# Kernel tuning notes

Hardware: AMD Instinct MI355X
Metric: run time of the kernel (lower is better)

Reference implementation:

```python
import jax, jax.numpy as jnp
import numpy as np

N = 50000      # nodes
E = 640000     # edges (before self loops)
IN = 128       # in_channels
H = 4          # heads (layer 1)
C = 64         # hidden_channels per head
OUT = 64       # out_channels
SLOPE = 0.2    # PyG GATConv default negative_slope


def setup_inputs() -> dict:
    key = jax.random.key(0)
    ks = jax.random.split(key, 12)
    x = jax.random.normal(ks[0], (N, IN), dtype=jnp.float32)
    edge_src = jax.random.randint(ks[1], (E,), 0, N, dtype=jnp.int32)
    edge_dst = jax.random.randint(ks[2], (E,), 0, N, dtype=jnp.int32)
    # Layer 1 params: Linear IN -> H*C, attention vectors a_src/a_dst [H, C], bias [H*C]
    W1 = jax.random.normal(ks[3], (IN, H * C), dtype=jnp.float32) / np.sqrt(IN)
    att_src1 = jax.random.normal(ks[4], (H, C), dtype=jnp.float32) / np.sqrt(C)
    att_dst1 = jax.random.normal(ks[5], (H, C), dtype=jnp.float32) / np.sqrt(C)
    b1 = jnp.zeros((H * C,), dtype=jnp.float32)
    # Layer 2 params: Linear H*C -> OUT, 1 head
    W2 = jax.random.normal(ks[6], (H * C, OUT), dtype=jnp.float32) / np.sqrt(H * C)
    att_src2 = jax.random.normal(ks[7], (1, OUT), dtype=jnp.float32) / np.sqrt(OUT)
    att_dst2 = jax.random.normal(ks[8], (1, OUT), dtype=jnp.float32) / np.sqrt(OUT)
    b2 = jnp.zeros((OUT,), dtype=jnp.float32)
    return {"x": x, "W1": W1, "att_src1": att_src1, "att_dst1": att_dst1, "b1": b1,
            "W2": W2, "att_src2": att_src2, "att_dst2": att_dst2, "b2": b2,
            "edge_src": edge_src, "edge_dst": edge_dst}


def gat_conv(x, src, dst, W, a_src, a_dst, b, heads, ch):
    """PyG GATConv (concat=True): gather -> LeakyReLU attention -> per-dst softmax -> scatter-add."""
    n = x.shape[0]
    h = (x @ W).reshape(n, heads, ch)                  # [N, H, C]
    al_s = jnp.sum(h * a_src, axis=-1)                 # [N, H] node-level src attention term
    al_d = jnp.sum(h * a_dst, axis=-1)                 # [N, H]
    e = jax.nn.leaky_relu(al_s[src] + al_d[dst], SLOPE)  # [E, H] edge scores
    m = jax.ops.segment_max(e, dst, num_segments=n)    # stable per-dst softmax
    ex = jnp.exp(e - m[dst])
    den = jax.ops.segment_sum(ex, dst, num_segments=n)
    alpha = ex / den[dst]                              # [E, H]
    msg = h[src] * alpha[:, :, None]                   # [E, H, C]
    out = jax.ops.segment_sum(msg, dst, num_segments=n)  # [N, H, C]
    return out.reshape(n, heads * ch) + b


def reference(x, W1, att_src1, att_dst1, b1, W2, att_src2, att_dst2, b2, edge_src, edge_dst):
    # PyG GATConv default add_self_loops=True
    loops = jnp.arange(N, dtype=edge_src.dtype)
    src = jnp.concatenate([edge_src, loops])
    dst = jnp.concatenate([edge_dst, loops])
    h = gat_conv(x, src, dst, W1, att_src1, att_dst1, b1, H, C)
    h = jax.nn.elu(h)                                  # F.elu; dropout p=0 -> no-op
    out = gat_conv(h, src, dst, W2, att_src2, att_dst2, b2, 1, OUT)
    return out
```

## Files before the change

kernel.cpp:

```cpp
#include <hip/hip_runtime.h>
#include <hip/hip_bf16.h>
#include <cstdint>
#include <cstddef>

#define N_NODES 50000
#define N_EDGES 640000
#define ET (N_EDGES + N_NODES)
#define IN_CH 128
#define H1 4
#define HC1 256
#define OUT_CH 64
#define SLOPE 0.2f
#define SCAN_NBLK ((N_NODES + 255) / 256)

typedef __attribute__((ext_vector_type(8))) short short8;
typedef __attribute__((ext_vector_type(4))) float floatx4;

__device__ __forceinline__ float bf2f(unsigned short u) {
    return __uint_as_float(((unsigned)u) << 16);
}
__device__ __forceinline__ unsigned short f2bf(float f) {
    unsigned u = __float_as_uint(f);
    unsigned r = 0x7fffu + ((u >> 16) & 1u);
    return (unsigned short)((u + r) >> 16);
}
__device__ __forceinline__ float ldf(const void* p, size_t i, bool f32) {
    return f32 ? ((const float*)p)[i] : bf2f(((const unsigned short*)p)[i]);
}

__global__ void detect_dtype(const unsigned short* __restrict__ x, unsigned* __restrict__ flag) {
    int lane = threadIdx.x & 63;
    int bad = 0;
    #pragma unroll
    for (int r = 0; r < 4; ++r) {
        float v = bf2f(x[r * 64 + lane]);
        if (!(v == v) || fabsf(v) > 1e4f) bad = 1;
    }
    unsigned long long m = __ballot(bad != 0);
    if (lane == 0) *flag = (m != 0ull) ? 1u : 0u;
}

#define XW (N_NODES * IN_CH / 8)
#define W1N (IN_CH * HC1)
#define W2N (HC1 * OUT_CH)
__global__ void conv_all(const void* __restrict__ x, const void* __restrict__ W1,
                         const void* __restrict__ W2, const unsigned* __restrict__ flag,
                         unsigned short* __restrict__ x16,
                         unsigned short* __restrict__ Wt1, unsigned short* __restrict__ Wt2)
{
    int i = blockIdx.x * blockDim.x + threadIdx.x;
    const bool f32 = (*flag != 0);
    if (i < XW) {
        size_t off = (size_t)i * 8;
        uint4 st;
        if (f32) {
            const float* xp = (const float*)x + off;
            float4 a = *(const float4*)xp;
            float4 b = *(const float4*)(xp + 4);
            st.x = (unsigned)f2bf(a.x) | ((unsigned)f2bf(a.y) << 16);
            st.y = (unsigned)f2bf(a.z) | ((unsigned)f2bf(a.w) << 16);
            st.z = (unsigned)f2bf(b.x) | ((unsigned)f2bf(b.y) << 16);
            st.w = (unsigned)f2bf(b.z) | ((unsigned)f2bf(b.w) << 16);
        } else {
            st = *(const uint4*)((const unsigned short*)x + off);
        }
        *(uint4*)(x16 + off) = st;
    } else if (i < XW + W1N) {
        int j = i - XW;
        int n = j / IN_CH, k = j % IN_CH;
        Wt1[j] = f2bf(ldf(W1, (size_t)k * HC1 + n, f32));
    } else if (i < XW + W1N + W2N) {
        int j = i - XW - W1N;
        int n = j / HC1, k = j % HC1;
        Wt2[j] = f2bf(ldf(W2, (size_t)k * OUT_CH + n, f32));
    }
}

__global__ void count_edges(const int* __restrict__ edst, int* __restrict__ counts)
{
    int i = blockIdx.x * blockDim.x + threadIdx.x;
    if (i >= ET) return;
    int d = (i < N_EDGES) ? edst[i] : (i - N_EDGES);
    atomicAdd(&counts[d], 1);
}

__global__ __launch_bounds__(256) void block_sums(
    const int* __restrict__ counts, int* __restrict__ bsum)
{
    int i = blockIdx.x * 256 + threadIdx.x;
    int v = (i < N_NODES) ? counts[i] : 0;
    #pragma unroll
    for (int off = 32; off > 0; off >>= 1) v += __shfl_down(v, off, 64);
    __shared__ int ws[4];
    int lane = threadIdx.x & 63, w = threadIdx.x >> 6;
    if (lane == 0) ws[w] = v;
    __syncthreads();
    if (threadIdx.x == 0) bsum[blockIdx.x] = ws[0] + ws[1] + ws[2] + ws[3];
}

__global__ __launch_bounds__(256) void scan_block_sums(
    const int* __restrict__ bsum, int* __restrict__ boff)
{
    __shared__ int s[256];
    int t = threadIdx.x;
    int v = (t < SCAN_NBLK) ? bsum[t] : 0;
    s[t] = v;
    __syncthreads();
    #pragma unroll
    for (int off = 1; off < 256; off <<= 1) {
        int u = (t >= off) ? s[t - off] : 0;
        __syncthreads();
        s[t] += u;
        __syncthreads();
    }
    if (t < SCAN_NBLK) boff[t] = s[t] - v;
}

__global__ __launch_bounds__(256) void write_rowptr(
    const int* __restrict__ counts, const int* __restrict__ boff,
    int* __restrict__ rowptr, int* __restrict__ cursor)
{
    __shared__ int s[256];
    int t = threadIdx.x;
    int i = blockIdx.x * 256 + t;
    int v = (i < N_NODES) ? counts[i] : 0;
    s[t] = v;
    __syncthreads();
    #pragma unroll
    for (int off = 1; off < 256; off <<= 1) {
        int u = (t >= off) ? s[t - off] : 0;
        __syncthreads();
        s[t] += u;
        __syncthreads();
    }
    if (i < N_NODES) {
        int r = boff[blockIdx.x] + s[t] - v;
        rowptr[i] = r; cursor[i] = r;
    }
    if (i == 0) rowptr[N_NODES] = ET;
}

__global__ void fill_csr(const int* __restrict__ esrc, const int* __restrict__ edst,
                         int* __restrict__ cursor, int* __restrict__ ecsr)
{
    int i = blockIdx.x * blockDim.x + threadIdx.x;
    if (i >= ET) return;
    int s = (i < N_EDGES) ? esrc[i] : (i - N_EDGES);
    int d = (i < N_EDGES) ? edst[i] : (i - N_EDGES);
    int pos = atomicAdd(&cursor[d], 1);
    ecsr[pos] = s;
}

template <int KK>
__global__ __launch_bounds__(256) void gemm_fused(
    const unsigned short* __restrict__ A,
    const unsigned short* __restrict__ Bt,
    const void* __restrict__ avs, const void* __restrict__ avd,
    const unsigned* __restrict__ flag,
    unsigned short* __restrict__ C,
    float* __restrict__ als, float* __restrict__ ald,
    int M, int N)
{
    const int tid = threadIdx.x;
    const int m0 = blockIdx.y * 64, n0 = blockIdx.x * 64;
    const int w = tid >> 6, lane = tid & 63;
    const int ln = lane & 15, quad = lane >> 4;
    const int m_frag = m0 + w * 16 + ln;
    floatx4 acc[4] = {{0.f,0.f,0.f,0.f},{0.f,0.f,0.f,0.f},{0.f,0.f,0.f,0.f},{0.f,0.f,0.f,0.f}};

    #pragma unroll
    for (int ks = 0; ks < KK / 32; ++ks) {
        const int kbase = ks * 32 + quad * 8;
        short8 a;
        if (m_frag < M) {
            a = *(const short8*)(A + (size_t)m_frag * KK + kbase);
        } else {
            #pragma unroll
            for (int j = 0; j < 8; ++j) a[j] = 0;
        }
        #pragma unroll
        for (int sub = 0; sub < 4; ++sub) {
            short8 b = *(const short8*)(Bt + (size_t)(n0 + sub * 16 + ln) * KK + kbase);
            acc[sub] = __builtin_amdgcn_mfma_f32_16x16x32_bf16(a, b, acc[sub], 0, 0, 0);
        }
    }

    #pragma unroll
    for (int sub = 0; sub < 4; ++sub) {
        #pragma unroll
        for (int r = 0; r < 4; ++r) {
            int m = m0 + w * 16 + quad * 4 + r;
            if (m < M)
                C[(size_t)m * N + n0 + sub * 16 + ln] = f2bf(acc[sub][r]);
        }
    }

    const bool f32in = (*flag != 0);
    float as[4], av[4];
    #pragma unroll
    for (int sub = 0; sub < 4; ++sub) {
        as[sub] = ldf(avs, n0 + sub * 16 + ln, f32in);
        av[sub] = ldf(avd, n0 + sub * 16 + ln, f32in);
    }
    const int Hh = N >> 6;
    #pragma unroll
    for (int r = 0; r < 4; ++r) {
        float ps = 0.f, pd = 0.f;
        #pragma unroll
        for (int sub = 0; sub < 4; ++sub) {
            ps += acc[sub][r] * as[sub];
            pd += acc[sub][r] * av[sub];
        }
        #pragma unroll
        for (int off = 1; off < 16; off <<= 1) {
            ps += __shfl_xor(ps, off, 64);
            pd += __shfl_xor(pd, off, 64);
        }
        int m = m0 + w * 16 + quad * 4 + r;
        if (ln == 0 && m < M) {
            als[(size_t)m * Hh + blockIdx.x] = ps;
            ald[(size_t)m * Hh + blockIdx.x] = pd;
        }
    }
}

__global__ __launch_bounds__(256) void agg_node1(
    const int* __restrict__ rowptr, const int* __restrict__ ecsr,
    const unsigned short* __restrict__ h, const float* __restrict__ als,
    const float* __restrict__ ald, const void* __restrict__ bias,
    const unsigned* __restrict__ flag, unsigned short* __restrict__ out)
{
    int wave = (blockIdx.x * blockDim.x + threadIdx.x) >> 6;
    int lane = threadIdx.x & 63;
    if (wave >= N_NODES) return;
    const int d = wave;
    const int hg = lane >> 4;
    const int c0 = (lane & 15) << 2;
    const int lo = rowptr[d], hi = rowptr[d + 1];
    const float ad = ald[d * H1 + hg];

    float acc0 = 0.f, acc1 = 0.f, acc2 = 0.f, acc3 = 0.f, den = 0.f;

    for (int eb = lo; eb < hi; eb += 8) {
        int s[8]; uint2 q[8]; float p[8];
        #pragma unroll
        for (int j = 0; j < 8; ++j) {
            int e = eb + j;
            s[j] = ecsr[(e < hi) ? e : (hi - 1)];
        }
        #pragma unroll
        for (int j = 0; j < 8; ++j)
            q[j] = *(const uint2*)(h + (size_t)s[j] * HC1 + hg * 64 + c0);
        #pragma unroll
        for (int j = 0; j < 8; ++j) {
            float t = als[s[j] * H1 + hg] + ad;
            t = (t > 0.f) ? t : SLOPE * t;
            float pv = __expf(t);
            p[j] = (eb + j < hi) ? pv : 0.f;
        }
        #pragma unroll
        for (int j = 0; j < 8; ++j) {
            den  += p[j];
            acc0 += p[j] * __uint_as_float(q[j].x << 16);
            acc1 += p[j] * __uint_as_float(q[j].x & 0xffff0000u);
            acc2 += p[j] * __uint_as_float(q[j].y << 16);
            acc3 += p[j] * __uint_as_float(q[j].y & 0xffff0000u);
        }
    }

    const bool f32in = (*flag != 0);
    const float inv = 1.f / den;
    float v0 = acc0 * inv + ldf(bias, hg * 64 + c0 + 0, f32in);
    float v1 = acc1 * inv + ldf(bias, hg * 64 + c0 + 1, f32in);
    float v2 = acc2 * inv + ldf(bias, hg * 64 + c0 + 2, f32in);
    float v3 = acc3 * inv + ldf(bias, hg * 64 + c0 + 3, f32in);
    v0 = (v0 > 0.f) ? v0 : (__expf(v0) - 1.f);
    v1 = (v1 > 0.f) ? v1 : (__expf(v1) - 1.f);
    v2 = (v2 > 0.f) ? v2 : (__expf(v2) - 1.f);
    v3 = (v3 > 0.f) ? v3 : (__expf(v3) - 1.f);
    uint2 st;
    st.x = (unsigned)f2bf(v0) | ((unsigned)f2bf(v1) << 16);
    st.y = (unsigned)f2bf(v2) | ((unsigned)f2bf(v3) << 16);
    *(uint2*)(out + (size_t)d * HC1 + hg * 64 + c0) = st;
}

__global__ __launch_bounds__(256) void agg_node2(
    const int* __restrict__ rowptr, const int* __restrict__ ecsr,
    const unsigned short* __restrict__ h, const float* __restrict__ als,
    const float* __restrict__ ald, const void* __restrict__ bias,
    const unsigned* __restrict__ flag, float* __restrict__ out)
{
    int wave = (blockIdx.x * blockDim.x + threadIdx.x) >> 6;
    int lane = threadIdx.x & 63;
    if (wave >= N_NODES) return;
    const int d = wave;
    const int eg = lane >> 3;
    const int c0 = (lane & 7) << 3;
    const int lo = rowptr[d], hi = rowptr[d + 1];
    const float ad = ald[d];

    float acc[8];
    #pragma unroll
    for (int j = 0; j < 8; ++j) acc[j] = 0.f;
    float den = 0.f;

    for (int eb = lo; eb < hi; eb += 8) {
        int e = eb + eg;
        if (e < hi) {
            int s = ecsr[e];
            uint4 q = *(const uint4*)(h + (size_t)s * OUT_CH + c0);
            float t = als[s] + ad;
            t = (t > 0.f) ? t : SLOPE * t;
            float p = __expf(t);
            den += p;
            acc[0] += p * __uint_as_float(q.x << 16);
            acc[1] += p * __uint_as_float(q.x & 0xffff0000u);
            acc[2] += p * __uint_as_float(q.y << 16);
            acc[3] += p * __uint_as_float(q.y & 0xffff0000u);
            acc[4] += p * __uint_as_float(q.z << 16);
            acc[5] += p * __uint_as_float(q.z & 0xffff0000u);
            acc[6] += p * __uint_as_float(q.w << 16);
            acc[7] += p * __uint_as_float(q.w & 0xffff0000u);
        }
    }
    #pragma unroll
    for (int off = 8; off <= 32; off <<= 1) {
        den += __shfl_xor(den, off, 64);
        #pragma unroll
        for (int j = 0; j < 8; ++j) acc[j] += __shfl_xor(acc[j], off, 64);
    }
    if (lane < 8) {
        const bool f32in = (*flag != 0);
        const float inv = 1.f / den;
        float4 v0, v1;
        v0.x = acc[0] * inv + ldf(bias, c0 + 0, f32in);
        v0.y = acc[1] * inv + ldf(bias, c0 + 1, f32in);
        v0.z = acc[2] * inv + ldf(bias, c0 + 2, f32in);
        v0.w = acc[3] * inv + ldf(bias, c0 + 3, f32in);
        v1.x = acc[4] * inv + ldf(bias, c0 + 4, f32in);
        v1.y = acc[5] * inv + ldf(bias, c0 + 5, f32in);
        v1.z = acc[6] * inv + ldf(bias, c0 + 6, f32in);
        v1.w = acc[7] * inv + ldf(bias, c0 + 7, f32in);
        *(float4*)(out + (size_t)d * OUT_CH + c0) = v0;
        *(float4*)(out + (size_t)d * OUT_CH + c0 + 4) = v1;
    }
}

extern "C" void kernel_launch(void* const* d_in, const int* in_sizes, int n_in,
                              void* d_out, int out_size, void* d_ws, size_t ws_size,
                              hipStream_t stream)
{
    const void* x   = d_in[0];
    const void* W1  = d_in[1];
    const void* as1 = d_in[2];
    const void* ad1 = d_in[3];
    const void* b1  = d_in[4];
    const void* W2  = d_in[5];
    const void* as2 = d_in[6];
    const void* ad2 = d_in[7];
    const void* b2  = d_in[8];
    const int* esrc = (const int*)d_in[9];
    const int* edst = (const int*)d_in[10];
    float* out = (float*)d_out;

    char* base = (char*)d_ws;
    const size_t MB = 1024 * 1024;
    unsigned short* x16  = (unsigned short*)(base);
    unsigned short* h16  = (unsigned short*)(base + 13 * MB);
    unsigned short* xo16 = (unsigned short*)(base + 39 * MB);
    unsigned short* h2   = (unsigned short*)(base + 65 * MB);
    float* als    = (float*)(base + 72 * MB);
    float* ald    = (float*)(base + 73 * MB);
    unsigned short* Wt1 = (unsigned short*)(base + 74 * MB);
    unsigned short* Wt2 = (unsigned short*)(base + 75 * MB);
    int* counts   = (int*)(base + 76 * MB);
    int* rowptr   = (int*)(base + 77 * MB);
    int* cursor   = (int*)(base + 78 * MB);
    int* ecsr     = (int*)(base + 79 * MB);
    int* bsum     = (int*)(base + 82 * MB);
    int* boff     = bsum + 256;
    unsigned* flag = (unsigned*)(base + 83 * MB);

    const int BLK = 256;
    const int edge_blocks = (ET + BLK - 1) / BLK;
    const int node_wave_blocks = (N_NODES * 64 + BLK - 1) / BLK;
    const int mtiles = (N_NODES + 63) / 64;

    detect_dtype<<<1, 64, 0, stream>>>((const unsigned short*)x, flag);

    (void)hipMemsetAsync(counts, 0, N_NODES * sizeof(int), stream);
    count_edges<<<edge_blocks, BLK, 0, stream>>>(edst, counts);
    block_sums<<<SCAN_NBLK, BLK, 0, stream>>>(counts, bsum);
    scan_block_sums<<<1, BLK, 0, stream>>>(bsum, boff);
    write_rowptr<<<SCAN_NBLK, BLK, 0, stream>>>(counts, boff, rowptr, cursor);
    fill_csr<<<edge_blocks, BLK, 0, stream>>>(esrc, edst, cursor, ecsr);

    conv_all<<<(XW + W1N + W2N + BLK - 1) / BLK, BLK, 0, stream>>>(
        x, W1, W2, flag, x16, Wt1, Wt2);

    {
        dim3 g(HC1 / 64, mtiles);
        gemm_fused<IN_CH><<<g, BLK, 0, stream>>>(x16, Wt1, as1, ad1, flag, h16, als, ald, N_NODES, HC1);
    }
    agg_node1<<<node_wave_blocks, BLK, 0, stream>>>(
        rowptr, ecsr, h16, als, ald, b1, flag, xo16);

    {
        dim3 g(OUT_CH / 64, mtiles);
        gemm_fused<HC1><<<g, BLK, 0, stream>>>(xo16, Wt2, as2, ad2, flag, h2, als, ald, N_NODES, OUT_CH);
    }
    agg_node2<<<node_wave_blocks, BLK, 0, stream>>>(
        rowptr, ecsr, h2, als, ald, b2, flag, out);
}
```

Baseline: 307.8 us.

## Merge preprocessing kernels and fold scan into one pass with inter-block spin

Cuts the launch count by merging independent work into shared grids. Dtype detection and the counts zeroing go into one init kernel, x/weight conversion is fused with edge counting, and the CSR fill is fused with the first GEMM. The three scan kernels become a single kernel where block 0 waits on an atomic counter, scans the block sums and releases the other blocks through a flag, which relies on all 196 blocks being co-resident. The layer-1 aggregation loop also changes from 8-wide clamped batches to 4-wide exact batches plus a scalar tail, dropping the wasted padded loads at the cost of less memory-level parallelism per iteration.

```diff
diff --git a/kernel.cpp b/kernel.cpp
--- a/kernel.cpp
+++ b/kernel.cpp
@@ -12,6 +12,13 @@
 #define OUT_CH 64
 #define SLOPE 0.2f
 #define SCAN_NBLK ((N_NODES + 255) / 256)
+#define XW (N_NODES * IN_CH / 8)
+#define W1N (IN_CH * HC1)
+#define W2N (HC1 * OUT_CH)
+#define CONVB ((XW + W1N + W2N + 255) / 256)
+#define EDGEB ((ET + 255) / 256)
+#define MT ((N_NODES + 63) / 64)
+#define G1B (4 * MT)
 
 typedef __attribute__((ext_vector_type(8))) short short8;
 typedef __attribute__((ext_vector_type(4))) float floatx4;
@@ -28,82 +35,84 @@
     return f32 ? ((const float*)p)[i] : bf2f(((const unsigned short*)p)[i]);
 }
 
-__global__ void detect_dtype(const unsigned short* __restrict__ x, unsigned* __restrict__ flag) {
-    int lane = threadIdx.x & 63;
-    int bad = 0;
-    #pragma unroll
-    for (int r = 0; r < 4; ++r) {
-        float v = bf2f(x[r * 64 + lane]);
-        if (!(v == v) || fabsf(v) > 1e4f) bad = 1;
-    }
-    unsigned long long m = __ballot(bad != 0);
-    if (lane == 0) *flag = (m != 0ull) ? 1u : 0u;
-}
-
-#define XW (N_NODES * IN_CH / 8)
-#define W1N (IN_CH * HC1)
-#define W2N (HC1 * OUT_CH)
-__global__ void conv_all(const void* __restrict__ x, const void* __restrict__ W1,
-                         const void* __restrict__ W2, const unsigned* __restrict__ flag,
-                         unsigned short* __restrict__ x16,
-                         unsigned short* __restrict__ Wt1, unsigned short* __restrict__ Wt2)
-{
-    int i = blockIdx.x * blockDim.x + threadIdx.x;
-    const bool f32 = (*flag != 0);
-    if (i < XW) {
-        size_t off = (size_t)i * 8;
-        uint4 st;
-        if (f32) {
-            const float* xp = (const float*)x + off;
-            float4 a = *(const float4*)xp;
-            float4 b = *(const float4*)(xp + 4);
-            st.x = (unsigned)f2bf(a.x) | ((unsigned)f2bf(a.y) << 16);
-            st.y = (unsigned)f2bf(a.z) | ((unsigned)f2bf(a.w) << 16);
-            st.z = (unsigned)f2bf(b.x) | ((unsigned)f2bf(b.y) << 16);
-            st.w = (unsigned)f2bf(b.z) | ((unsigned)f2bf(b.w) << 16);
-        } else {
-            st = *(const uint4*)((const unsigned short*)x + off);
-        }
-        *(uint4*)(x16 + off) = st;
-    } else if (i < XW + W1N) {
-        int j = i - XW;
-        int n = j / IN_CH, k = j % IN_CH;
-        Wt1[j] = f2bf(ldf(W1, (size_t)k * HC1 + n, f32));
-    } else if (i < XW + W1N + W2N) {
-        int j = i - XW - W1N;
-        int n = j / HC1, k = j % HC1;
-        Wt2[j] = f2bf(ldf(W2, (size_t)k * OUT_CH + n, f32));
-    }
-}
-
-__global__ void count_edges(const int* __restrict__ edst, int* __restrict__ counts)
-{
-    int i = blockIdx.x * blockDim.x + threadIdx.x;
-    if (i >= ET) return;
-    int d = (i < N_EDGES) ? edst[i] : (i - N_EDGES);
-    atomicAdd(&counts[d], 1);
-}
-
-__global__ __launch_bounds__(256) void block_sums(
-    const int* __restrict__ counts, int* __restrict__ bsum)
-{
-    int i = blockIdx.x * 256 + threadIdx.x;
+__global__ __launch_bounds__(256) void init_all(
+    const unsigned short* __restrict__ x, unsigned* __restrict__ flag,
+    int* __restrict__ counts, int* __restrict__ state)
+{
+    int b = blockIdx.x;
+    if (b < SCAN_NBLK) {
+        int i = b * 256 + threadIdx.x;
+        if (i < N_NODES) counts[i] = 0;
+    } else {
+        int t = threadIdx.x;
+        if (t < 64) {
+            int bad = 0;
+            #pragma unroll
+            for (int r = 0; r < 4; ++r) {
+                float v = bf2f(x[r * 64 + t]);
+                if (!(v == v) || fabsf(v) > 1e4f) bad = 1;
+            }
+            unsigned long long m = __ballot(bad != 0);
+            if (t == 0) *flag = (m != 0ull) ? 1u : 0u;
+        } else if (t == 64) {
+            state[0] = 0; state[1] = 0;
+        }
+    }
+}
+
+__global__ __launch_bounds__(256) void conv_count(
+    const void* __restrict__ x, const void* __restrict__ W1,
+    const void* __restrict__ W2, const unsigned* __restrict__ flag,
+    unsigned short* __restrict__ x16,
+    unsigned short* __restrict__ Wt1, unsigned short* __restrict__ Wt2,
+    const int* __restrict__ edst, int* __restrict__ counts)
+{
+    int b = blockIdx.x;
+    if (b < CONVB) {
+        int i = b * 256 + threadIdx.x;
+        const bool f32 = (*flag != 0);
+        if (i < XW) {
+            size_t off = (size_t)i * 8;
+            uint4 st;
+            if (f32) {
+                const float* xp = (const float*)x + off;
+                float4 a = *(const float4*)xp;
+                float4 c = *(const float4*)(xp + 4);
+                st.x = (unsigned)f2bf(a.x) | ((unsigned)f2bf(a.y) << 16);
+                st.y = (unsigned)f2bf(a.z) | ((unsigned)f2bf(a.w) << 16);
+                st.z = (unsigned)f2bf(c.x) | ((unsigned)f2bf(c.y) << 16);
+                st.w = (unsigned)f2bf(c.z) | ((unsigned)f2bf(c.w) << 16);
+            } else {
+                st = *(const uint4*)((const unsigned short*)x + off);
+            }
+            *(uint4*)(x16 + off) = st;
+        } else if (i < XW + W1N) {
+            int j = i - XW;
+            int n = j / IN_CH, k = j % IN_CH;
+            Wt1[j] = f2bf(ldf(W1, (size_t)k * HC1 + n, f32));
+        } else if (i < XW + W1N + W2N) {
+            int j = i - XW - W1N;
+            int n = j / HC1, k = j % HC1;
+            Wt2[j] = f2bf(ldf(W2, (size_t)k * OUT_CH + n, f32));
+        }
+    } else {
+        int i = (b - CONVB) * 256 + threadIdx.x;
+        if (i < ET) {
+            int d = (i < N_EDGES) ? edst[i] : (i - N_EDGES);
+            atomicAdd(&counts[d], 1);
+        }
+    }
+}
+
+__global__ __launch_bounds__(256) void scan_onepass(
+    const int* __restrict__ counts, int* __restrict__ rowptr,
+    int* __restrict__ cursor, int* __restrict__ bsum,
+    int* __restrict__ boff, int* __restrict__ state)
+{
+    __shared__ int s[256];
+    const int t = threadIdx.x, b = blockIdx.x;
+    const int i = b * 256 + t;
     int v = (i < N_NODES) ? counts[i] : 0;
-    #pragma unroll
-    for (int off = 32; off > 0; off >>= 1) v += __shfl_down(v, off, 64);
-    __shared__ int ws[4];
-    int lane = threadIdx.x & 63, w = threadIdx.x >> 6;
-    if (lane == 0) ws[w] = v;
-    __syncthreads();
-    if (threadIdx.x == 0) bsum[blockIdx.x] = ws[0] + ws[1] + ws[2] + ws[3];
-}
-
-__global__ __launch_bounds__(256) void scan_block_sums(
-    const int* __restrict__ bsum, int* __restrict__ boff)
-{
-    __shared__ int s[256];
-    int t = threadIdx.x;
-    int v = (t < SCAN_NBLK) ? bsum[t] : 0;
     s[t] = v;
     __syncthreads();
     #pragma unroll
@@ -113,56 +122,57 @@
         s[t] += u;
         __syncthreads();
     }
-    if (t < SCAN_NBLK) boff[t] = s[t] - v;
-}
-
-__global__ __launch_bounds__(256) void write_rowptr(
-    const int* __restrict__ counts, const int* __restrict__ boff,
-    int* __restrict__ rowptr, int* __restrict__ cursor)
-{
-    __shared__ int s[256];
-    int t = threadIdx.x;
-    int i = blockIdx.x * 256 + t;
-    int v = (i < N_NODES) ? counts[i] : 0;
-    s[t] = v;
+    const int incl = s[t];
+    if (t == 255) {
+        __hip_atomic_store(&bsum[b], incl, __ATOMIC_RELAXED, __HIP_MEMORY_SCOPE_AGENT);
+        __hip_atomic_fetch_add(&state[0], 1, __ATOMIC_ACQ_REL, __HIP_MEMORY_SCOPE_AGENT);
+    }
+    if (b == 0) {
+        if (t == 0) {
+            while (__hip_atomic_load(&state[0], __ATOMIC_ACQUIRE, __HIP_MEMORY_SCOPE_AGENT) < SCAN_NBLK)
+                __builtin_amdgcn_s_sleep(8);
+        }
+        __syncthreads();
+        int w = (t < SCAN_NBLK)
+              ? __hip_atomic_load(&bsum[t], __ATOMIC_RELAXED, __HIP_MEMORY_SCOPE_AGENT) : 0;
+        s[t] = w;
+        __syncthreads();
+        #pragma unroll
+        for (int off = 1; off < 256; off <<= 1) {
+            int u = (t >= off) ? s[t - off] : 0;
+            __syncthreads();
+            s[t] += u;
+            __syncthreads();
+        }
+        if (t < SCAN_NBLK)
+            __hip_atomic_store(&boff[t], s[t] - w, __ATOMIC_RELAXED, __HIP_MEMORY_SCOPE_AGENT);
+        __syncthreads();
+        if (t == 0)
+            __hip_atomic_store(&state[1], 1, __ATOMIC_RELEASE, __HIP_MEMORY_SCOPE_AGENT);
+    }
+    if (t == 0) {
+        while (__hip_atomic_load(&state[1], __ATOMIC_ACQUIRE, __HIP_MEMORY_SCOPE_AGENT) == 0)
+            __builtin_amdgcn_s_sleep(8);
+    }
     __syncthreads();
-    #pragma unroll
-    for (int off = 1; off < 256; off <<= 1) {
-        int u = (t >= off) ? s[t - off] : 0;
-        __syncthreads();
-        s[t] += u;
-        __syncthreads();
-    }
+    int off0 = __hip_atomic_load(&boff[b], __ATOMIC_RELAXED, __HIP_MEMORY_SCOPE_AGENT);
     if (i < N_NODES) {
-        int r = boff[blockIdx.x] + s[t] - v;
+        int r = off0 + incl - v;
         rowptr[i] = r; cursor[i] = r;
     }
     if (i == 0) rowptr[N_NODES] = ET;
 }
 
-__global__ void fill_csr(const int* __restrict__ esrc, const int* __restrict__ edst,
-                         int* __restrict__ cursor, int* __restrict__ ecsr)
-{
-    int i = blockIdx.x * blockDim.x + threadIdx.x;
-    if (i >= ET) return;
-    int s = (i < N_EDGES) ? esrc[i] : (i - N_EDGES);
-    int d = (i < N_EDGES) ? edst[i] : (i - N_EDGES);
-    int pos = atomicAdd(&cursor[d], 1);
-    ecsr[pos] = s;
-}
-
 template <int KK>
-__global__ __launch_bounds__(256) void gemm_fused(
-    const unsigned short* __restrict__ A,
-    const unsigned short* __restrict__ Bt,
+__device__ __forceinline__ void gemm_body(
+    const unsigned short* __restrict__ A, const unsigned short* __restrict__ Bt,
     const void* __restrict__ avs, const void* __restrict__ avd,
-    const unsigned* __restrict__ flag,
-    unsigned short* __restrict__ C,
+    const unsigned* __restrict__ flag, unsigned short* __restrict__ C,
     float* __restrict__ als, float* __restrict__ ald,
-    int M, int N)
+    int M, int N, int bx, int by)
 {
     const int tid = threadIdx.x;
-    const int m0 = blockIdx.y * 64, n0 = blockIdx.x * 64;
+    const int m0 = by * 64, n0 = bx * 64;
     const int w = tid >> 6, lane = tid & 63;
     const int ln = lane & 15, quad = lane >> 4;
     const int m_frag = m0 + w * 16 + ln;
@@ -218,10 +228,43 @@
         }
         int m = m0 + w * 16 + quad * 4 + r;
         if (ln == 0 && m < M) {
-            als[(size_t)m * Hh + blockIdx.x] = ps;
-            ald[(size_t)m * Hh + blockIdx.x] = pd;
-        }
-    }
+            als[(size_t)m * Hh + bx] = ps;
+            ald[(size_t)m * Hh + bx] = pd;
+        }
+    }
+}
+
+__global__ __launch_bounds__(256) void gemm1_fill(
+    const unsigned short* __restrict__ x16, const unsigned short* __restrict__ Wt1,
+    const void* __restrict__ as1, const void* __restrict__ ad1,
+    const unsigned* __restrict__ flag, unsigned short* __restrict__ h16,
+    float* __restrict__ als, float* __restrict__ ald,
+    const int* __restrict__ esrc, const int* __restrict__ edst,
+    int* __restrict__ cursor, int* __restrict__ ecsr)
+{
+    int b = blockIdx.x;
+    if (b < G1B) {
+        gemm_body<IN_CH>(x16, Wt1, as1, ad1, flag, h16, als, ald,
+                         N_NODES, HC1, b & 3, b >> 2);
+    } else {
+        int i = (b - G1B) * 256 + threadIdx.x;
+        if (i < ET) {
+            int s = (i < N_EDGES) ? esrc[i] : (i - N_EDGES);
+            int d = (i < N_EDGES) ? edst[i] : (i - N_EDGES);
+            int pos = atomicAdd(&cursor[d], 1);
+            ecsr[pos] = s;
+        }
+    }
+}
+
+__global__ __launch_bounds__(256) void gemm2(
+    const unsigned short* __restrict__ xo16, const unsigned short* __restrict__ Wt2,
+    const void* __restrict__ as2, const void* __restrict__ ad2,
+    const unsigned* __restrict__ flag, unsigned short* __restrict__ h2,
+    float* __restrict__ als, float* __restrict__ ald)
+{
+    gemm_body<HC1>(xo16, Wt2, as2, ad2, flag, h2, als, ald,
+                   N_NODES, OUT_CH, 0, blockIdx.x);
 }
 
 __global__ __launch_bounds__(256) void agg_node1(
@@ -241,31 +284,43 @@
 
     float acc0 = 0.f, acc1 = 0.f, acc2 = 0.f, acc3 = 0.f, den = 0.f;
 
-    for (int eb = lo; eb < hi; eb += 8) {
-        int s[8]; uint2 q[8]; float p[8];
-        #pragma unroll
-        for (int j = 0; j < 8; ++j) {
-            int e = eb + j;
-            s[j] = ecsr[(e < hi) ? e : (hi - 1)];
-        }
-        #pragma unroll
-        for (int j = 0; j < 8; ++j)
-            q[j] = *(const uint2*)(h + (size_t)s[j] * HC1 + hg * 64 + c0);
-        #pragma unroll
-        for (int j = 0; j < 8; ++j) {
-            float t = als[s[j] * H1 + hg] + ad;
-            t = (t > 0.f) ? t : SLOPE * t;
-            float pv = __expf(t);
-            p[j] = (eb + j < hi) ? pv : 0.f;
-        }
-        #pragma unroll
-        for (int j = 0; j < 8; ++j) {
-            den  += p[j];
-            acc0 += p[j] * __uint_as_float(q[j].x << 16);
-            acc1 += p[j] * __uint_as_float(q[j].x & 0xffff0000u);
-            acc2 += p[j] * __uint_as_float(q[j].y << 16);
-            acc3 += p[j] * __uint_as_float(q[j].y & 0xffff0000u);
-        }
+    int e = lo;
+    for (; e + 3 < hi; e += 4) {
+        int s0 = ecsr[e], s1 = ecsr[e + 1], s2 = ecsr[e + 2], s3 = ecsr[e + 3];
+        uint2 q0 = *(const uint2*)(h + (size_t)s0 * HC1 + hg * 64 + c0);
+        uint2 q1 = *(const uint2*)(h + (size_t)s1 * HC1 + hg * 64 + c0);
+        uint2 q2 = *(const uint2*)(h + (size_t)s2 * HC1 + hg * 64 + c0);
+        uint2 q3 = *(const uint2*)(h + (size_t)s3 * HC1 + hg * 64 + c0);
+        float t0 = als[s0 * H1 + hg] + ad;
+        float t1 = als[s1 * H1 + hg] + ad;
+        float t2 = als[s2 * H1 + hg] + ad;
+        float t3 = als[s3 * H1 + hg] + ad;
+        t0 = (t0 > 0.f) ? t0 : SLOPE * t0;
+        t1 = (t1 > 0.f) ? t1 : SLOPE * t1;
+        t2 = (t2 > 0.f) ? t2 : SLOPE * t2;
+        t3 = (t3 > 0.f) ? t3 : SLOPE * t3;
+        float p0 = __expf(t0), p1 = __expf(t1), p2 = __expf(t2), p3 = __expf(t3);
+        den += (p0 + p1) + (p2 + p3);
+        acc0 += p0 * __uint_as_float(q0.x << 16)         + p1 * __uint_as_float(q1.x << 16)
+              + p2 * __uint_as_float(q2.x << 16)         + p3 * __uint_as_float(q3.x << 16);
+        acc1 += p0 * __uint_as_float(q0.x & 0xffff0000u) + p1 * __uint_as_float(q1.x & 0xffff0000u)
+              + p2 * __uint_as_float(q2.x & 0xffff0000u) + p3 * __uint_as_float(q3.x & 0xffff0000u);
+        acc2 += p0 * __uint_as_float(q0.y << 16)         + p1 * __uint_as_float(q1.y << 16)
+              + p2 * __uint_as_float(q2.y << 16)         + p3 * __uint_as_float(q3.y << 16);
+        acc3 += p0 * __uint_as_float(q0.y & 0xffff0000u) + p1 * __uint_as_float(q1.y & 0xffff0000u)
+              + p2 * __uint_as_float(q2.y & 0xffff0000u) + p3 * __uint_as_float(q3.y & 0xffff0000u);
+    }
+    for (; e < hi; ++e) {
+        int s0 = ecsr[e];
+        uint2 q0 = *(const uint2*)(h + (size_t)s0 * HC1 + hg * 64 + c0);
+        float t0 = als[s0 * H1 + hg] + ad;
+        t0 = (t0 > 0.f) ? t0 : SLOPE * t0;
+        float p0 = __expf(t0);
+        den += p0;
+        acc0 += p0 * __uint_as_float(q0.x << 16);
+        acc1 += p0 * __uint_as_float(q0.x & 0xffff0000u);
+        acc2 += p0 * __uint_as_float(q0.y << 16);
+        acc3 += p0 * __uint_as_float(q0.y & 0xffff0000u);
     }
 
     const bool f32in = (*flag != 0);
@@ -379,36 +434,29 @@
     int* ecsr     = (int*)(base + 79 * MB);
     int* bsum     = (int*)(base + 82 * MB);
     int* boff     = bsum + 256;
+    int* state    = boff + 256;
     unsigned* flag = (unsigned*)(base + 83 * MB);
 
     const int BLK = 256;
-    const int edge_blocks = (ET + BLK - 1) / BLK;
     const int node_wave_blocks = (N_NODES * 64 + BLK - 1) / BLK;
-    const int mtiles = (N_NODES + 63) / 64;
-
-    detect_dtype<<<1, 64, 0, stream>>>((const unsigned short*)x, flag);
-
-    (void)hipMemsetAsync(counts, 0, N_NODES * sizeof(int), stream);
-    count_edges<<<edge_blocks, BLK, 0, stream>>>(edst, counts);
-    block_sums<<<SCAN_NBLK, BLK, 0, stream>>>(counts, bsum);
-    scan_block_sums<<<1, BLK, 0, stream>>>(bsum, boff);
-    write_rowptr<<<SCAN_NBLK, BLK, 0, stream>>>(counts, boff, rowptr, cursor);
-    fill_csr<<<edge_blocks, BLK, 0, stream>>>(esrc, edst, cursor, ecsr);
-
-    conv_all<<<(XW + W1N + W2N + BLK - 1) / BLK, BLK, 0, stream>>>(
-        x, W1, W2, flag, x16, Wt1, Wt2);
-
-    {
-        dim3 g(HC1 / 64, mtiles);
-        gemm_fused<IN_CH><<<g, BLK, 0, stream>>>(x16, Wt1, as1, ad1, flag, h16, als, ald, N_NODES, HC1);
-    }
+
+    init_all<<<SCAN_NBLK + 1, BLK, 0, stream>>>(
+        (const unsigned short*)x, flag, counts, state);
+
+    conv_count<<<CONVB + EDGEB, BLK, 0, stream>>>(
+        x, W1, W2, flag, x16, Wt1, Wt2, edst, counts);
+
+    scan_onepass<<<SCAN_NBLK, BLK, 0, stream>>>(
+        counts, rowptr, cursor, bsum, boff, state);
+
+    gemm1_fill<<<G1B + EDGEB, BLK, 0, stream>>>(
+        x16, Wt1, as1, ad1, flag, h16, als, ald, esrc, edst, cursor, ecsr);
+
     agg_node1<<<node_wave_blocks, BLK, 0, stream>>>(
         rowptr, ecsr, h16, als, ald, b1, flag, xo16);
 
-    {
-        dim3 g(OUT_CH / 64, mtiles);
-        gemm_fused<HC1><<<g, BLK, 0, stream>>>(xo16, Wt2, as2, ad2, flag, h2, als, ald, N_NODES, OUT_CH);
-    }
+    gemm2<<<MT, BLK, 0, stream>>>(xo16, Wt2, as2, ad2, flag, h2, als, ald);
+
     agg_node2<<<node_wave_blocks, BLK, 0, stream>>>(
         rowptr, ecsr, h2, als, ald, b2, flag, out);
 }
```

Result: no change. 304.1 us (-1.2%).
